# Performance work log

Measured on AMD Instinct MI355X. Metric: run time of the kernel, lower is better.

## Reference

```python
import jax, jax.numpy as jnp
import numpy as np

B, N, D = 2, 2048, 1024
H, WS = 16, 128  # num_heads, window_size
DH = D // H
HALF = WS // 2  # window is [i-HALF, i+HALF] inclusive -> 129 keys interior


def setup_inputs() -> dict:
    key = jax.random.key(0)
    ks = jax.random.split(key, 5)
    return {
        "x": jax.random.normal(ks[0], (B, N, D), dtype=jnp.float32),
        "Wqkv": jax.random.normal(ks[1], (D, 3 * D), dtype=jnp.float32) * 0.02,
        "bqkv": jax.random.normal(ks[2], (3 * D,), dtype=jnp.float32) * 0.02,
        "Wout": jax.random.normal(ks[3], (D, D), dtype=jnp.float32) * 0.02,
        "bout": jax.random.normal(ks[4], (D,), dtype=jnp.float32) * 0.02,
    }


def reference(x, Wqkv, bqkv, Wout, bout):
    b, n, d = x.shape
    scale = DH ** -0.5
    qkv = x @ Wqkv + bqkv  # [b, n, 3d]
    q, k, v = jnp.split(qkv, 3, axis=-1)
    # [b, n, d] -> [b, h, n, dh]
    def heads(t):
        return t.reshape(b, n, H, DH).transpose(0, 2, 1, 3)
    q, k, v = heads(q), heads(k), heads(v)
    scores = jnp.einsum("bhid,bhjd->bhij", q, k) * scale  # [b, h, n, n]
    # per-token window [max(0,i-HALF), min(n,i+HALF+1)) == |i-j| <= HALF
    idx = jnp.arange(n)
    band = jnp.abs(idx[:, None] - idx[None, :]) <= HALF  # [n, n]
    neg = jnp.asarray(jnp.finfo(scores.dtype).min, scores.dtype)
    scores = jnp.where(band[None, None], scores, neg)
    attn = jax.nn.softmax(scores, axis=-1)
    out = jnp.einsum("bhij,bhjd->bhid", attn, v)  # [b, h, n, dh]
    out = out.transpose(0, 2, 1, 3).reshape(b, n, d)
    return out @ Wout + bout
```

## Files before the change

kernel.cpp:

```cpp
#include <hip/hip_runtime.h>
#include <hip/hip_bf16.h>
#include <cstdint>
#include <cstddef>

#define BB 2
#define NN 2048
#define DD 1024
#define HH 16
#define DHH 64
#define SCALE 0.125f

typedef _Float16 f16x8 __attribute__((ext_vector_type(8)));
typedef _Float16 f16x4 __attribute__((ext_vector_type(4)));
typedef float f32x4 __attribute__((ext_vector_type(4)));

#define AS1(p) ((__attribute__((address_space(1))) void*)(p))
#define AS3(p) ((__attribute__((address_space(3))) void*)(p))

__global__ __launch_bounds__(256) void prep(const float* __restrict__ x, _Float16* __restrict__ x_h,
                                            const float* __restrict__ Wqkv, _Float16* __restrict__ Wqkv_t,
                                            const float* __restrict__ Wout, _Float16* __restrict__ Wout_t) {
    __shared__ float tile[32][33];
    int bx = blockIdx.x, tid = threadIdx.x;
    if (bx < 2048) {
        int i = bx * 2048 + tid * 8;
        f32x4 a = *(const f32x4*)(x + i);
        f32x4 b = *(const f32x4*)(x + i + 4);
        f16x8 o;
        o[0] = (_Float16)a[0]; o[1] = (_Float16)a[1]; o[2] = (_Float16)a[2]; o[3] = (_Float16)a[3];
        o[4] = (_Float16)b[0]; o[5] = (_Float16)b[1]; o[6] = (_Float16)b[2]; o[7] = (_Float16)b[3];
        *(f16x8*)(x_h + i) = o;
        return;
    }
    const float* in; _Float16* out; int C, tc, tr;
    if (bx < 5120) { int t = bx - 2048; C = 3 * DD; in = Wqkv; out = Wqkv_t; tc = t % 96; tr = t / 96; }
    else           { int t = bx - 5120; C = DD;     in = Wout; out = Wout_t; tc = t % 32; tr = t / 32; }
    int R = DD;
    int txx = tid & 31, ty = tid >> 5;
    int r0 = tr * 32, c0 = tc * 32;
#pragma unroll
    for (int i = 0; i < 32; i += 8)
        tile[ty + i][txx] = in[(size_t)(r0 + ty + i) * C + (c0 + txx)];
    __syncthreads();
#pragma unroll
    for (int i = 0; i < 32; i += 8)
        out[(size_t)(c0 + ty + i) * R + (r0 + txx)] = (_Float16)tile[txx][ty + i];
}

__global__ __launch_bounds__(256) void gemm_qkv(const _Float16* __restrict__ A,
                                                const _Float16* __restrict__ Bt,
                                                const float* __restrict__ bias,
                                                _Float16* __restrict__ q_h,
                                                _Float16* __restrict__ k_h,
                                                _Float16* __restrict__ vt_h) {
    const int K = DD, M = BB * NN;
    __shared__ __align__(16) _Float16 As[128 * 64];
    __shared__ __align__(16) _Float16 Bs[128 * 64];
    int tid = threadIdx.x;
    int wave = tid >> 6, lane = tid & 63;
    int bm = blockIdx.y * 128, bn = blockIdx.x * 128;
    int wm = (wave >> 1) * 64, wn = (wave & 1) * 64;
    int lhi = lane >> 4, llo = lane & 15;
    (void)M;

    f32x4 acc[4][4] = {};

    int srow = wave * 32 + (lane >> 3);
    int scol = ((lane & 7) ^ (lane >> 3)) * 8;
    const _Float16* gA = A + (size_t)(bm + srow) * K + scol;
    const _Float16* gB = Bt + (size_t)(bn + srow) * K + scol;
    _Float16* lA = As + wave * 2048 + lane * 8;
    _Float16* lB = Bs + wave * 2048 + lane * 8;

    for (int k0 = 0; k0 < K; k0 += 64) {
        __syncthreads();
#pragma unroll
        for (int p = 0; p < 4; ++p) {
            __builtin_amdgcn_global_load_lds(AS1(gA + (size_t)p * 8 * K + k0), AS3(lA + p * 512), 16, 0, 0);
            __builtin_amdgcn_global_load_lds(AS1(gB + (size_t)p * 8 * K + k0), AS3(lB + p * 512), 16, 0, 0);
        }
        __syncthreads();

#pragma unroll
        for (int ks = 0; ks < 2; ++ks) {
            f16x8 af[4], bf[4];
            int swz = (((ks * 4 + lhi) ^ (llo & 7)) * 8);
#pragma unroll
            for (int mt = 0; mt < 4; ++mt)
                af[mt] = *(const f16x8*)(As + (wm + mt * 16 + llo) * 64 + swz);
#pragma unroll
            for (int nt = 0; nt < 4; ++nt)
                bf[nt] = *(const f16x8*)(Bs + (wn + nt * 16 + llo) * 64 + swz);
#pragma unroll
            for (int mt = 0; mt < 4; ++mt)
#pragma unroll
                for (int nt = 0; nt < 4; ++nt)
                    acc[mt][nt] = __builtin_amdgcn_mfma_f32_16x16x32_f16(af[mt], bf[nt], acc[mt][nt], 0, 0, 0);
        }
    }

    int region = bn >> 10;
#pragma unroll
    for (int nt = 0; nt < 4; ++nt) {
        int col = bn + wn + nt * 16 + llo;
        float bv = bias[col];
        int c = col & 1023;
#pragma unroll
        for (int mt = 0; mt < 4; ++mt) {
            int row = bm + wm + mt * 16 + lhi * 4;
            int b = row >> 11, n = row & 2047;
            if (region == 2) {
                int h = c >> 6, dh = c & 63;
                f16x4 v4;
#pragma unroll
                for (int r = 0; r < 4; ++r) v4[r] = (_Float16)(acc[mt][nt][r] + bv);
                *(f16x4*)(vt_h + ((size_t)((b * HH + h) * DHH + dh)) * NN + n) = v4;
            } else {
                _Float16* dst = (region == 0 ? q_h : k_h) + ((size_t)(b * NN + n)) * DD + c;
#pragma unroll
                for (int r = 0; r < 4; ++r)
                    dst[(size_t)r * DD] = (_Float16)(acc[mt][nt][r] + bv);
            }
        }
    }
}

template <int BM>
__global__ __launch_bounds__(256) void gemm_f16_bt(const _Float16* __restrict__ A,
                                                   const _Float16* __restrict__ Bt,
                                                   const float* __restrict__ bias,
                                                   float* __restrict__ Cf,
                                                   int M, int N, int K) {
    constexpr int MT = BM / 32;
    constexpr int AP = BM / 32;
    __shared__ __align__(16) _Float16 As[BM * 64];
    __shared__ __align__(16) _Float16 Bs[128 * 64];
    int tid = threadIdx.x;
    int wave = tid >> 6, lane = tid & 63;
    int bm = blockIdx.y * BM, bn = blockIdx.x * 128;
    int wm = (wave >> 1) * (BM / 2), wn = (wave & 1) * 64;
    int lhi = lane >> 4, llo = lane & 15;

    f32x4 acc[MT][4] = {};

    int srowA = wave * (BM / 4) + (lane >> 3);
    int srowB = wave * 32 + (lane >> 3);
    int scol = ((lane & 7) ^ (lane >> 3)) * 8;
    const _Float16* gA = A + (size_t)(bm + srowA) * K + scol;
    const _Float16* gB = Bt + (size_t)(bn + srowB) * K + scol;
    _Float16* lA = As + wave * (AP * 512) + lane * 8;
    _Float16* lB = Bs + wave * 2048 + lane * 8;

    for (int k0 = 0; k0 < K; k0 += 64) {
        __syncthreads();
#pragma unroll
        for (int p = 0; p < AP; ++p)
            __builtin_amdgcn_global_load_lds(AS1(gA + (size_t)p * 8 * K + k0), AS3(lA + p * 512), 16, 0, 0);
#pragma unroll
        for (int p = 0; p < 4; ++p)
            __builtin_amdgcn_global_load_lds(AS1(gB + (size_t)p * 8 * K + k0), AS3(lB + p * 512), 16, 0, 0);
        __syncthreads();

#pragma unroll
        for (int ks = 0; ks < 2; ++ks) {
            f16x8 af[MT], bf[4];
            int swz = (((ks * 4 + lhi) ^ (llo & 7)) * 8);
#pragma unroll
            for (int mt = 0; mt < MT; ++mt)
                af[mt] = *(const f16x8*)(As + (wm + mt * 16 + llo) * 64 + swz);
#pragma unroll
            for (int nt = 0; nt < 4; ++nt)
                bf[nt] = *(const f16x8*)(Bs + (wn + nt * 16 + llo) * 64 + swz);
#pragma unroll
            for (int mt = 0; mt < MT; ++mt)
#pragma unroll
                for (int nt = 0; nt < 4; ++nt)
                    acc[mt][nt] = __builtin_amdgcn_mfma_f32_16x16x32_f16(af[mt], bf[nt], acc[mt][nt], 0, 0, 0);
        }
    }

#pragma unroll
    for (int nt = 0; nt < 4; ++nt) {
        int col = bn + wn + nt * 16 + llo;
        float bv = bias[col];
#pragma unroll
        for (int mt = 0; mt < MT; ++mt) {
#pragma unroll
            for (int r = 0; r < 4; ++r) {
                int row = bm + wm + mt * 16 + lhi * 4 + r;
                Cf[(size_t)row * N + col] = acc[mt][nt][r] + bv;
            }
        }
    }
}

#define KP 64
#define PP 200
#define VP 200
__global__ __launch_bounds__(256) void local_attn(const _Float16* __restrict__ q_h,
                                                  const _Float16* __restrict__ k_h,
                                                  const _Float16* __restrict__ vt_h,
                                                  _Float16* __restrict__ outh) {
    __shared__ __align__(16) _Float16 Ks[192 * KP];
    __shared__ __align__(16) _Float16 Ps[64 * PP];
    __shared__ __align__(16) _Float16 Vt[64 * VP];
    int tid = threadIdx.x;
    int i0 = blockIdx.x * 64;
    int h = blockIdx.y, b = blockIdx.z;

    int wave = tid >> 6, lane = tid & 63;
    int llo = lane & 15, lhi = lane >> 4;

    {
        int srow = lane >> 3;
        int chunk = ((lane & 7) ^ (lane >> 3)) * 8;
        const _Float16* kb = k_h + (size_t)(b * NN) * DD + h * DHH + chunk;
#pragma unroll
        for (int q = 0; q < 6; ++q) {
            int p = wave * 6 + q;
            int j = i0 - 64 + p * 8 + srow;
            __builtin_amdgcn_global_load_lds(AS1(kb + (ptrdiff_t)j * DD), AS3(Ks + p * 512 + lane * 8), 16, 0, 0);
        }
    }

    {
        const _Float16* vb = vt_h + (size_t)((b * HH + h) * DHH) * NN + (i0 - 64);
        for (int u = tid; u < 1536; u += 256) {
            int d = u / 24, c = u % 24;
            f16x8 vv = *(const f16x8*)(vb + (ptrdiff_t)d * NN + c * 8);
            *(f16x8*)(Vt + d * VP + c * 8) = vv;
        }
    }

    int qrow = wave * 16 + llo;
    int qi = i0 + qrow;
    const _Float16* qp = q_h + (size_t)(b * NN + qi) * DD + h * DHH;
    f16x8 qf0 = *(const f16x8*)(qp + lhi * 8);
    f16x8 qf1 = *(const f16x8*)(qp + 32 + lhi * 8);
    __syncthreads();

    float sc[12][4];
#pragma unroll
    for (int mt = 0; mt < 12; ++mt) {
        const _Float16* kr = Ks + (mt * 16 + llo) * 64;
        f16x8 kf0 = *(const f16x8*)(kr + ((lhi ^ (llo & 7)) * 8));
        f16x8 kf1 = *(const f16x8*)(kr + (((lhi + 4) ^ (llo & 7)) * 8));
        f32x4 a = {0.f, 0.f, 0.f, 0.f};
        a = __builtin_amdgcn_mfma_f32_16x16x32_f16(kf0, qf0, a, 0, 0, 0);
        a = __builtin_amdgcn_mfma_f32_16x16x32_f16(kf1, qf1, a, 0, 0, 0);
#pragma unroll
        for (int r = 0; r < 4; ++r) sc[mt][r] = a[r];
    }

    float m = -1e30f;
#pragma unroll
    for (int mt = 0; mt < 12; ++mt)
#pragma unroll
        for (int r = 0; r < 4; ++r) {
            int sidx = mt * 16 + lhi * 4 + r;
            int j = i0 - 64 + sidx;
            int dj = j - qi;
            bool valid = (j >= 0) && (j < NN) && (dj <= 64) && (dj >= -64);
            float v = valid ? sc[mt][r] * SCALE : -1e30f;
            sc[mt][r] = v;
            m = fmaxf(m, v);
        }
    m = fmaxf(m, __shfl_xor(m, 16, 64));
    m = fmaxf(m, __shfl_xor(m, 32, 64));
    float l = 0.f;
#pragma unroll
    for (int mt = 0; mt < 12; ++mt)
#pragma unroll
        for (int r = 0; r < 4; ++r) {
            float e = __expf(sc[mt][r] - m);
            sc[mt][r] = e;
            l += e;
        }
    l += __shfl_xor(l, 16, 64);
    l += __shfl_xor(l, 32, 64);
    float invl = 1.f / l;

#pragma unroll
    for (int mt = 0; mt < 12; ++mt) {
        f16x4 pv;
#pragma unroll
        for (int r = 0; r < 4; ++r) pv[r] = (_Float16)(sc[mt][r] * invl);
        *(f16x4*)(Ps + qrow * PP + mt * 16 + lhi * 4) = pv;
    }
    __asm__ volatile("s_waitcnt lgkmcnt(0)" ::: "memory");

    f32x4 oacc[4] = {};
#pragma unroll
    for (int ks = 0; ks < 6; ++ks) {
        f16x8 pf = *(const f16x8*)(Ps + (wave * 16 + llo) * PP + ks * 32 + lhi * 8);
#pragma unroll
        for (int nt = 0; nt < 4; ++nt) {
            f16x8 vf = *(const f16x8*)(Vt + (nt * 16 + llo) * VP + ks * 32 + lhi * 8);
            oacc[nt] = __builtin_amdgcn_mfma_f32_16x16x32_f16(pf, vf, oacc[nt], 0, 0, 0);
        }
    }

    _Float16* orow = outh + (size_t)(b * NN) * DD + h * DHH;
#pragma unroll
    for (int nt = 0; nt < 4; ++nt)
#pragma unroll
        for (int r = 0; r < 4; ++r) {
            int q = wave * 16 + lhi * 4 + r;
            int d = nt * 16 + llo;
            orow[(size_t)(i0 + q) * DD + d] = (_Float16)oacc[nt][r];
        }
}

extern "C" void kernel_launch(void* const* d_in, const int* in_sizes, int n_in,
                              void* d_out, int out_size, void* d_ws, size_t ws_size,
                              hipStream_t stream) {
    const float* x    = (const float*)d_in[0];
    const float* Wqkv = (const float*)d_in[1];
    const float* bqkv = (const float*)d_in[2];
    const float* Wout = (const float*)d_in[3];
    const float* bout = (const float*)d_in[4];
    float* out = (float*)d_out;

    char* ws = (char*)d_ws;
    _Float16* x_h    = (_Float16*)(ws);
    _Float16* Wqkv_t = (_Float16*)(ws + (size_t)8  * 1024 * 1024);
    _Float16* Wout_t = (_Float16*)(ws + (size_t)14 * 1024 * 1024);
    _Float16* q_h    = (_Float16*)(ws + (size_t)16 * 1024 * 1024);
    _Float16* k_h    = (_Float16*)(ws + (size_t)24 * 1024 * 1024);
    _Float16* vt_h   = (_Float16*)(ws + (size_t)32 * 1024 * 1024);
    _Float16* attn_h = (_Float16*)(ws + (size_t)40 * 1024 * 1024);

    int M = BB * NN;

    prep<<<6144, 256, 0, stream>>>(x, x_h, Wqkv, Wqkv_t, Wout, Wout_t);

    gemm_qkv<<<dim3((3 * DD) / 128, M / 128), 256, 0, stream>>>(
        x_h, Wqkv_t, bqkv, q_h, k_h, vt_h);

    local_attn<<<dim3(NN / 64, HH, BB), 256, 0, stream>>>(q_h, k_h, vt_h, attn_h);

    gemm_f16_bt<64><<<dim3(DD / 128, M / 64), 256, 0, stream>>>(
        attn_h, Wout_t, bout, out, M, DD, DD);
}
```

Baseline: 162.5 us.

## Remap blocks per XCD for L2 locality and vectorize GEMM epilogue stores via swapped MFMA operands

After: 156.8 us. -3.5%, faster.

```diff
diff --git a/kernel.cpp b/kernel.cpp
--- a/kernel.cpp
+++ b/kernel.cpp
@@ -47,21 +47,67 @@
         out[(size_t)(c0 + ty + i) * R + (r0 + txx)] = (_Float16)tile[txx][ty + i];
 }
 
+template <bool SWAP, int MT>
+__device__ __forceinline__ void gemm_kloop(const _Float16* __restrict__ gA,
+                                           const _Float16* __restrict__ gB,
+                                           _Float16* lA, _Float16* lB,
+                                           const _Float16* As, const _Float16* Bs,
+                                           int wm, int wn, int llo, int lhi, int K,
+                                           f32x4 acc[][MT > 4 ? MT : 4]) {
+    for (int k0 = 0; k0 < K; k0 += 64) {
+        __syncthreads();
+#pragma unroll
+        for (int p = 0; p < MT; ++p)
+            __builtin_amdgcn_global_load_lds(AS1(gA + (size_t)p * 8 * K + k0), AS3(lA + p * 512), 16, 0, 0);
+#pragma unroll
+        for (int p = 0; p < 4; ++p)
+            __builtin_amdgcn_global_load_lds(AS1(gB + (size_t)p * 8 * K + k0), AS3(lB + p * 512), 16, 0, 0);
+        __syncthreads();
+
+#pragma unroll
+        for (int ks = 0; ks < 2; ++ks) {
+            f16x8 af[MT], bf[4];
+            int swz = (((ks * 4 + lhi) ^ (llo & 7)) * 8);
+#pragma unroll
+            for (int mt = 0; mt < MT; ++mt)
+                af[mt] = *(const f16x8*)(As + (wm + mt * 16 + llo) * 64 + swz);
+#pragma unroll
+            for (int nt = 0; nt < 4; ++nt)
+                bf[nt] = *(const f16x8*)(Bs + (wn + nt * 16 + llo) * 64 + swz);
+            if (SWAP) {
+#pragma unroll
+                for (int nt = 0; nt < 4; ++nt)
+#pragma unroll
+                    for (int mt = 0; mt < MT; ++mt)
+                        acc[nt][mt] = __builtin_amdgcn_mfma_f32_16x16x32_f16(bf[nt], af[mt], acc[nt][mt], 0, 0, 0);
+            } else {
+#pragma unroll
+                for (int mt = 0; mt < MT; ++mt)
+#pragma unroll
+                    for (int nt = 0; nt < 4; ++nt)
+                        acc[mt][nt] = __builtin_amdgcn_mfma_f32_16x16x32_f16(af[mt], bf[nt], acc[mt][nt], 0, 0, 0);
+            }
+        }
+    }
+}
+
 __global__ __launch_bounds__(256) void gemm_qkv(const _Float16* __restrict__ A,
                                                 const _Float16* __restrict__ Bt,
                                                 const float* __restrict__ bias,
                                                 _Float16* __restrict__ q_h,
                                                 _Float16* __restrict__ k_h,
                                                 _Float16* __restrict__ vt_h) {
-    const int K = DD, M = BB * NN;
+    const int K = DD;
     __shared__ __align__(16) _Float16 As[128 * 64];
     __shared__ __align__(16) _Float16 Bs[128 * 64];
+    int id = blockIdx.x;
+    int xcd = id & 7, j = id >> 3;
+    int bn = (xcd * 3 + j % 3) * 128;
+    int bm = (j / 3) * 128;
     int tid = threadIdx.x;
     int wave = tid >> 6, lane = tid & 63;
-    int bm = blockIdx.y * 128, bn = blockIdx.x * 128;
     int wm = (wave >> 1) * 64, wn = (wave & 1) * 64;
     int lhi = lane >> 4, llo = lane & 15;
-    (void)M;
 
     f32x4 acc[4][4] = {};
 
@@ -72,124 +118,86 @@
     _Float16* lA = As + wave * 2048 + lane * 8;
     _Float16* lB = Bs + wave * 2048 + lane * 8;
 
-    for (int k0 = 0; k0 < K; k0 += 64) {
-        __syncthreads();
-#pragma unroll
-        for (int p = 0; p < 4; ++p) {
-            __builtin_amdgcn_global_load_lds(AS1(gA + (size_t)p * 8 * K + k0), AS3(lA + p * 512), 16, 0, 0);
-            __builtin_amdgcn_global_load_lds(AS1(gB + (size_t)p * 8 * K + k0), AS3(lB + p * 512), 16, 0, 0);
-        }
-        __syncthreads();
-
-#pragma unroll
-        for (int ks = 0; ks < 2; ++ks) {
-            f16x8 af[4], bf[4];
-            int swz = (((ks * 4 + lhi) ^ (llo & 7)) * 8);
-#pragma unroll
-            for (int mt = 0; mt < 4; ++mt)
-                af[mt] = *(const f16x8*)(As + (wm + mt * 16 + llo) * 64 + swz);
-#pragma unroll
-            for (int nt = 0; nt < 4; ++nt)
-                bf[nt] = *(const f16x8*)(Bs + (wn + nt * 16 + llo) * 64 + swz);
-#pragma unroll
-            for (int mt = 0; mt < 4; ++mt)
-#pragma unroll
-                for (int nt = 0; nt < 4; ++nt)
-                    acc[mt][nt] = __builtin_amdgcn_mfma_f32_16x16x32_f16(af[mt], bf[nt], acc[mt][nt], 0, 0, 0);
-        }
-    }
-
     int region = bn >> 10;
-#pragma unroll
-    for (int nt = 0; nt < 4; ++nt) {
-        int col = bn + wn + nt * 16 + llo;
-        float bv = bias[col];
-        int c = col & 1023;
-#pragma unroll
-        for (int mt = 0; mt < 4; ++mt) {
-            int row = bm + wm + mt * 16 + lhi * 4;
-            int b = row >> 11, n = row & 2047;
-            if (region == 2) {
-                int h = c >> 6, dh = c & 63;
+    if (region == 2) {
+        gemm_kloop<false, 4>(gA, gB, lA, lB, As, Bs, wm, wn, llo, lhi, K, acc);
+#pragma unroll
+        for (int nt = 0; nt < 4; ++nt) {
+            int col = bn + wn + nt * 16 + llo;
+            float bv = bias[col];
+            int c = col & 1023;
+            int h = c >> 6, dh = c & 63;
+#pragma unroll
+            for (int mt = 0; mt < 4; ++mt) {
+                int row = bm + wm + mt * 16 + lhi * 4;
+                int b = row >> 11, n = row & 2047;
                 f16x4 v4;
 #pragma unroll
                 for (int r = 0; r < 4; ++r) v4[r] = (_Float16)(acc[mt][nt][r] + bv);
                 *(f16x4*)(vt_h + ((size_t)((b * HH + h) * DHH + dh)) * NN + n) = v4;
-            } else {
-                _Float16* dst = (region == 0 ? q_h : k_h) + ((size_t)(b * NN + n)) * DD + c;
-#pragma unroll
-                for (int r = 0; r < 4; ++r)
-                    dst[(size_t)r * DD] = (_Float16)(acc[mt][nt][r] + bv);
             }
         }
-    }
-}
-
-template <int BM>
-__global__ __launch_bounds__(256) void gemm_f16_bt(const _Float16* __restrict__ A,
-                                                   const _Float16* __restrict__ Bt,
-                                                   const float* __restrict__ bias,
-                                                   float* __restrict__ Cf,
-                                                   int M, int N, int K) {
-    constexpr int MT = BM / 32;
-    constexpr int AP = BM / 32;
-    __shared__ __align__(16) _Float16 As[BM * 64];
+    } else {
+        gemm_kloop<true, 4>(gA, gB, lA, lB, As, Bs, wm, wn, llo, lhi, K, acc);
+        _Float16* dst0 = (region == 0 ? q_h : k_h);
+#pragma unroll
+        for (int nt = 0; nt < 4; ++nt) {
+            int cbase = bn + wn + nt * 16 + lhi * 4;
+            f32x4 b4 = *(const f32x4*)(bias + cbase);
+            int c = cbase & 1023;
+#pragma unroll
+            for (int mt = 0; mt < 4; ++mt) {
+                int t = bm + wm + mt * 16 + llo;
+                int b = t >> 11, n = t & 2047;
+                f16x4 v4;
+#pragma unroll
+                for (int r = 0; r < 4; ++r) v4[r] = (_Float16)(acc[nt][mt][r] + b4[r]);
+                *(f16x4*)(dst0 + (size_t)(b * NN + n) * DD + c) = v4;
+            }
+        }
+    }
+}
+
+__global__ __launch_bounds__(256) void gemm_out(const _Float16* __restrict__ A,
+                                                const _Float16* __restrict__ Bt,
+                                                const float* __restrict__ bias,
+                                                float* __restrict__ Cf) {
+    const int K = DD, N = DD;
+    __shared__ __align__(16) _Float16 As[64 * 64];
     __shared__ __align__(16) _Float16 Bs[128 * 64];
+    int id = blockIdx.x;
+    int xcd = id & 7, j = id >> 3;
+    int bm = (xcd * 8 + (j >> 3)) * 64;
+    int bn = (j & 7) * 128;
     int tid = threadIdx.x;
     int wave = tid >> 6, lane = tid & 63;
-    int bm = blockIdx.y * BM, bn = blockIdx.x * 128;
-    int wm = (wave >> 1) * (BM / 2), wn = (wave & 1) * 64;
+    int wm = (wave >> 1) * 32, wn = (wave & 1) * 64;
     int lhi = lane >> 4, llo = lane & 15;
 
-    f32x4 acc[MT][4] = {};
-
-    int srowA = wave * (BM / 4) + (lane >> 3);
+    f32x4 acc[4][4] = {};
+
+    int srowA = wave * 16 + (lane >> 3);
     int srowB = wave * 32 + (lane >> 3);
     int scol = ((lane & 7) ^ (lane >> 3)) * 8;
     const _Float16* gA = A + (size_t)(bm + srowA) * K + scol;
     const _Float16* gB = Bt + (size_t)(bn + srowB) * K + scol;
-    _Float16* lA = As + wave * (AP * 512) + lane * 8;
+    _Float16* lA = As + wave * 1024 + lane * 8;
     _Float16* lB = Bs + wave * 2048 + lane * 8;
 
-    for (int k0 = 0; k0 < K; k0 += 64) {
-        __syncthreads();
-#pragma unroll
-        for (int p = 0; p < AP; ++p)
-            __builtin_amdgcn_global_load_lds(AS1(gA + (size_t)p * 8 * K + k0), AS3(lA + p * 512), 16, 0, 0);
-#pragma unroll
-        for (int p = 0; p < 4; ++p)
-            __builtin_amdgcn_global_load_lds(AS1(gB + (size_t)p * 8 * K + k0), AS3(lB + p * 512), 16, 0, 0);
-        __syncthreads();
-
-#pragma unroll
-        for (int ks = 0; ks < 2; ++ks) {
-            f16x8 af[MT], bf[4];
-            int swz = (((ks * 4 + lhi) ^ (llo & 7)) * 8);
-#pragma unroll
-            for (int mt = 0; mt < MT; ++mt)
-                af[mt] = *(const f16x8*)(As + (wm + mt * 16 + llo) * 64 + swz);
-#pragma unroll
-            for (int nt = 0; nt < 4; ++nt)
-                bf[nt] = *(const f16x8*)(Bs + (wn + nt * 16 + llo) * 64 + swz);
-#pragma unroll
-            for (int mt = 0; mt < MT; ++mt)
-#pragma unroll
-                for (int nt = 0; nt < 4; ++nt)
-                    acc[mt][nt] = __builtin_amdgcn_mfma_f32_16x16x32_f16(af[mt], bf[nt], acc[mt][nt], 0, 0, 0);
-        }
-    }
+    gemm_kloop<true, 2>(gA, gB, lA, lB, As, Bs, wm, wn, llo, lhi, K,
+                        (f32x4(*)[4])acc);
 
 #pragma unroll
     for (int nt = 0; nt < 4; ++nt) {
-        int col = bn + wn + nt * 16 + llo;
-        float bv = bias[col];
-#pragma unroll
-        for (int mt = 0; mt < MT; ++mt) {
-#pragma unroll
-            for (int r = 0; r < 4; ++r) {
-                int row = bm + wm + mt * 16 + lhi * 4 + r;
-                Cf[(size_t)row * N + col] = acc[mt][nt][r] + bv;
-            }
+        int cbase = bn + wn + nt * 16 + lhi * 4;
+        f32x4 b4 = *(const f32x4*)(bias + cbase);
+#pragma unroll
+        for (int mt = 0; mt < 2; ++mt) {
+            int t = bm + wm + mt * 16 + llo;
+            f32x4 v4;
+#pragma unroll
+            for (int r = 0; r < 4; ++r) v4[r] = acc[nt][mt][r] + b4[r];
+            *(f32x4*)(Cf + (size_t)t * N + cbase) = v4;
         }
     }
 }
@@ -205,8 +213,11 @@
     __shared__ __align__(16) _Float16 Ps[64 * PP];
     __shared__ __align__(16) _Float16 Vt[64 * VP];
     int tid = threadIdx.x;
-    int i0 = blockIdx.x * 64;
-    int h = blockIdx.y, b = blockIdx.z;
+    int id = blockIdx.x;
+    int xcd = id & 7, j = id >> 3;
+    int i0 = (xcd * 4 + (j & 3)) * 64;
+    int hb = j >> 2;
+    int h = hb & 15, b = hb >> 4;
 
     int wave = tid >> 6, lane = tid & 63;
     int llo = lane & 15, lhi = lane >> 4;
@@ -218,8 +229,8 @@
 #pragma unroll
         for (int q = 0; q < 6; ++q) {
             int p = wave * 6 + q;
-            int j = i0 - 64 + p * 8 + srow;
-            __builtin_amdgcn_global_load_lds(AS1(kb + (ptrdiff_t)j * DD), AS3(Ks + p * 512 + lane * 8), 16, 0, 0);
+            int jj = i0 - 64 + p * 8 + srow;
+            __builtin_amdgcn_global_load_lds(AS1(kb + (ptrdiff_t)jj * DD), AS3(Ks + p * 512 + lane * 8), 16, 0, 0);
         }
     }
 
@@ -258,9 +269,9 @@
 #pragma unroll
         for (int r = 0; r < 4; ++r) {
             int sidx = mt * 16 + lhi * 4 + r;
-            int j = i0 - 64 + sidx;
-            int dj = j - qi;
-            bool valid = (j >= 0) && (j < NN) && (dj <= 64) && (dj >= -64);
+            int jj = i0 - 64 + sidx;
+            int dj = jj - qi;
+            bool valid = (jj >= 0) && (jj < NN) && (dj <= 64) && (dj >= -64);
             float v = valid ? sc[mt][r] * SCALE : -1e30f;
             sc[mt][r] = v;
             m = fmaxf(m, v);
@@ -330,15 +341,11 @@
     _Float16* vt_h   = (_Float16*)(ws + (size_t)32 * 1024 * 1024);
     _Float16* attn_h = (_Float16*)(ws + (size_t)40 * 1024 * 1024);
 
-    int M = BB * NN;
-
     prep<<<6144, 256, 0, stream>>>(x, x_h, Wqkv, Wqkv_t, Wout, Wout_t);
 
-    gemm_qkv<<<dim3((3 * DD) / 128, M / 128), 256, 0, stream>>>(
-        x_h, Wqkv_t, bqkv, q_h, k_h, vt_h);
-
-    local_attn<<<dim3(NN / 64, HH, BB), 256, 0, stream>>>(q_h, k_h, vt_h, attn_h);
-
-    gemm_f16_bt<64><<<dim3(DD / 128, M / 64), 256, 0, stream>>>(
-        attn_h, Wout_t, bout, out, M, DD, DD);
-}
+    gemm_qkv<<<768, 256, 0, stream>>>(x_h, Wqkv_t, bqkv, q_h, k_h, vt_h);
+
+    local_attn<<<1024, 256, 0, stream>>>(q_h, k_h, vt_h, attn_h);
+
+    gemm_out<<<512, 256, 0, stream>>>(attn_h, Wout_t, bout, out);
+}
```
